# Performance work log

Measured on AMD Instinct MI355X. Metric: run time of the kernel, lower is better.

The kernel has to match this reference:

```python
import jax, jax.numpy as jnp
import numpy as np
import math

HIDDEN = 2048
N_HEADS = 16
HEAD_DIM = HIDDEN // N_HEADS  # 128
ROPE_THETA = 10000.0


def _rope_cos_sin(seq_len, dim, theta, dtype):
    # Megatron RotaryEmbedding: freqs = pos \outer inv_freq; emb = cat(freqs, freqs)
    inv_freq = 1.0 / (theta ** (jnp.arange(0, dim, 2, dtype=jnp.float32) / dim))
    pos = jnp.arange(seq_len, dtype=jnp.float32)
    freqs = jnp.outer(pos, inv_freq)            # [S, dim/2]
    emb = jnp.concatenate([freqs, freqs], -1)   # [S, dim]
    return jnp.cos(emb).astype(dtype), jnp.sin(emb).astype(dtype)


def _rotate_half(x):
    half = x.shape[-1] // 2
    return jnp.concatenate([-x[..., half:], x[..., :half]], axis=-1)


def setup_inputs() -> dict:
    key = jax.random.key(0)
    k1, k2, k3 = jax.random.split(key, 3)
    B, S = 2, 2048
    hidden_states = jax.random.normal(k1, (B, S, HIDDEN), dtype=jnp.float32)
    # torch Linear weights are [out_features, in_features]
    w_qkv = jax.random.normal(k2, (3 * HIDDEN, HIDDEN), dtype=jnp.float32) * (1.0 / math.sqrt(HIDDEN))
    w_o = jax.random.normal(k3, (HIDDEN, HIDDEN), dtype=jnp.float32) * (1.0 / math.sqrt(HIDDEN))
    return {"hidden_states": hidden_states, "w_qkv": w_qkv, "w_o": w_o}


def reference(hidden_states, w_qkv, w_o):
    B, S, H = hidden_states.shape
    # fused QKV projection: [B,S,H] @ [H, 3H] -> view (.., n_heads, 3, head_dim)
    mixed = jnp.einsum('bsh,oh->bso', hidden_states, w_qkv)
    mixed = mixed.reshape(B, S, N_HEADS, 3, HEAD_DIM)
    q, k, v = mixed[..., 0, :], mixed[..., 1, :], mixed[..., 2, :]  # [B,S,Hn,D]

    # fused split + RoPE (full rotary dim = head_dim)
    cos, sin = _rope_cos_sin(S, HEAD_DIM, ROPE_THETA, hidden_states.dtype)
    cos = cos[None, :, None, :]  # [1,S,1,D]
    sin = sin[None, :, None, :]
    q = q * cos + _rotate_half(q) * sin
    k = k * cos + _rotate_half(k) * sin

    # causal scaled-dot-product attention (flash_attn_func equivalent math)
    scale = 1.0 / math.sqrt(HEAD_DIM)
    scores = jnp.einsum('bqhd,bkhd->bhqk', q, k) * scale  # [B,Hn,S,S]
    causal = jnp.tril(jnp.ones((S, S), dtype=bool))
    scores = jnp.where(causal[None, None], scores, jnp.finfo(scores.dtype).min)
    probs = jax.nn.softmax(scores, axis=-1)
    attn = jnp.einsum('bhqk,bkhd->bqhd', probs, v)  # [B,S,Hn,D]

    attn = attn.reshape(B, S, H)
    out = jnp.einsum('bsh,oh->bso', attn, w_o)
    return out
```

## Files before the change

kernel.cpp:

```cpp
#include <hip/hip_runtime.h>
#include <hip/hip_bf16.h>
#include <cstdint>
#include <cstddef>

#define S_DIM 2048
#define H_DIM 2048
#define NHEAD 16
#define HD_DIM 128
#define O3    6144
#define BS    4096
#define NBH   32

typedef short  s16x4  __attribute__((ext_vector_type(4)));
typedef short  s16x8  __attribute__((ext_vector_type(8)));
typedef __bf16 bf16x8 __attribute__((ext_vector_type(8)));
typedef float  f32x4  __attribute__((ext_vector_type(4)));

__device__ __forceinline__ unsigned short f2bf(float f) {
  unsigned int b = __float_as_uint(f);
  b += 0x7FFFu + ((b >> 16) & 1u);
  return (unsigned short)(b >> 16);
}
__device__ __forceinline__ float bf2f(unsigned short u) {
  return __uint_as_float(((unsigned int)u) << 16);
}
__device__ __forceinline__ bf16x8 load8(const unsigned short* p) {
  s16x8 r = *(const s16x8*)p;
  return __builtin_bit_cast(bf16x8, r);
}
__device__ __forceinline__ f32x4 mfma_bf16(bf16x8 a, bf16x8 b, f32x4 c) {
  return __builtin_amdgcn_mfma_f32_16x16x32_bf16(a, b, c, 0, 0, 0);
}
__device__ __forceinline__ void gload_lds16(const void* g, void* l) {
  __builtin_amdgcn_global_load_lds(
      (__attribute__((address_space(1))) unsigned int*)g,
      (__attribute__((address_space(3))) unsigned int*)l, 16, 0, 0);
}

__global__ void prep_kernel(const float* __restrict__ hid,
                            const float* __restrict__ wqkv,
                            const float* __restrict__ wo,
                            unsigned short* __restrict__ hid_b,
                            unsigned short* __restrict__ wqkv_b,
                            unsigned short* __restrict__ wo_b,
                            float* __restrict__ cosT,
                            float* __restrict__ sinT) {
  const int nA = 2097152, nB = 3145728, nC = 1048576, nD = 131072;
  const int total = nA + nB + nC + nD;
  int stride = gridDim.x * blockDim.x;
  for (int i = blockIdx.x * blockDim.x + threadIdx.x; i < total; i += stride) {
    if (i < nA + nB + nC) {
      const float* src; unsigned short* dst; int j;
      if (i < nA)            { src = hid;  dst = hid_b;  j = i; }
      else if (i < nA + nB)  { src = wqkv; dst = wqkv_b; j = i - nA; }
      else                   { src = wo;   dst = wo_b;   j = i - nA - nB; }
      float4 v = ((const float4*)src)[j];
      ushort4 o;
      o.x = f2bf(v.x); o.y = f2bf(v.y); o.z = f2bf(v.z); o.w = f2bf(v.w);
      ((ushort4*)dst)[j] = o;
    } else {
      int idx = i - nA - nB - nC;
      int s = idx >> 6, d = idx & 63;
      float inv = expf(-((float)d / 64.0f) * 9.210340371976184f);
      float ang = (float)s * inv;
      float sn, cs;
      sincosf(ang, &sn, &cs);
      cosT[idx] = cs;
      sinT[idx] = sn;
    }
  }
}

template <bool OUT_BF16, bool QKV_MAP>
__global__ __launch_bounds__(512, 1)
void gemm3b_kernel(const unsigned short* __restrict__ A,
                   const unsigned short* __restrict__ Bw,
                   void* __restrict__ C, int M, int N, int K) {
  __shared__ __align__(16) unsigned short lA[3][128 * 64];
  __shared__ __align__(16) unsigned short lB[3][256 * 64];
  const int tid  = threadIdx.x;
  const int wave = tid >> 6, lane = tid & 63;
  const int wm = wave >> 2, wn = wave & 3;
  const int lg = lane >> 4, ll = lane & 15;

  const int nbx = gridDim.x;
  const int id  = blockIdx.y * nbx + blockIdx.x;
  int m_tile, n_tile;
  if (QKV_MAP) {
    const int k = id & 7, q = id >> 3;
    const int ng = q >> 5, r = q & 31;
    m_tile = (k >> 1) * 8 + (r & 7);
    n_tile = (k & 1) * 12 + ng * 4 + (r >> 3);
  } else {
    const int nwg = gridDim.x * gridDim.y;
    const int swz = (id & 7) * (nwg >> 3) + (id >> 3);
    m_tile = swz / nbx;
    n_tile = swz % nbx;
  }
  const int m0 = m_tile * 128, n0 = n_tile * 256;

  f32x4 acc[4][4];
#pragma unroll
  for (int i = 0; i < 4; ++i)
#pragma unroll
    for (int j = 0; j < 4; ++j) acc[i][j] = (f32x4){0.f, 0.f, 0.f, 0.f};

  const unsigned short* aP[2];
  const unsigned short* bP[4];
  int aD[2], bD[4];
#pragma unroll
  for (int i = 0; i < 2; ++i) {
    int cb = (i * 8 + wave) * 64 + lane;
    int cs = cb ^ ((cb >> 3) & 7);
    aP[i] = A + (size_t)(m0 + (cs >> 3)) * K + (cs & 7) * 8;
    aD[i] = cb * 8;
  }
#pragma unroll
  for (int i = 0; i < 4; ++i) {
    int cb = (i * 8 + wave) * 64 + lane;
    int cs = cb ^ ((cb >> 3) & 7);
    bP[i] = Bw + (size_t)(n0 + (cs >> 3)) * K + (cs & 7) * 8;
    bD[i] = cb * 8;
  }

  auto STAGE = [&](int buf, int t) {
    const int kt = t << 6;
#pragma unroll
    for (int i = 0; i < 2; ++i) gload_lds16(aP[i] + kt, &lA[buf][aD[i]]);
#pragma unroll
    for (int i = 0; i < 4; ++i) gload_lds16(bP[i] + kt, &lB[buf][bD[i]]);
  };

  const int NT = K >> 6;
  STAGE(0, 0);
  if (NT > 1) {
    STAGE(1, 1);
    asm volatile("s_waitcnt vmcnt(6)" ::: "memory");
  } else {
    asm volatile("s_waitcnt vmcnt(0)" ::: "memory");
  }
  asm volatile("s_barrier" ::: "memory");

  for (int t = 0; t < NT; ++t) {
    const int cur = t % 3;
    const char* lAc = (const char*)&lA[cur][0];
    const char* lBc = (const char*)&lB[cur][0];

    bf16x8 af[4][2], bfr[2][2][2];
#pragma unroll
    for (int fq = 0; fq < 4; ++fq) {
      int r = wm * 64 + fq * 16 + ll;
#pragma unroll
      for (int kk = 0; kk < 2; ++kk) {
        int a = (r * 128 + kk * 64 + lg * 16) ^ ((r & 7) << 4);
        af[fq][kk] = load8((const unsigned short*)(lAc + a));
      }
    }
#pragma unroll
    for (int nh = 0; nh < 2; ++nh)
#pragma unroll
      for (int fq = 0; fq < 2; ++fq) {
        int r = wn * 64 + nh * 32 + fq * 16 + ll;
#pragma unroll
        for (int kk = 0; kk < 2; ++kk) {
          int a = (r * 128 + kk * 64 + lg * 16) ^ ((r & 7) << 4);
          bfr[nh][fq][kk] = load8((const unsigned short*)(lBc + a));
        }
      }

    if (t + 2 < NT) STAGE((t + 2) % 3, t + 2);

    __builtin_amdgcn_s_setprio(1);
#pragma unroll
    for (int nh = 0; nh < 2; ++nh)
#pragma unroll
      for (int fq = 0; fq < 4; ++fq)
#pragma unroll
        for (int gq = 0; gq < 2; ++gq)
#pragma unroll
          for (int kk = 0; kk < 2; ++kk)
            acc[fq][nh * 2 + gq] =
                mfma_bf16(af[fq][kk], bfr[nh][gq][kk], acc[fq][nh * 2 + gq]);
    __builtin_amdgcn_s_setprio(0);

    if (t + 2 < NT)
      asm volatile("s_waitcnt vmcnt(6)" ::: "memory");
    else if (t + 1 < NT)
      asm volatile("s_waitcnt vmcnt(0)" ::: "memory");
    asm volatile("s_barrier" ::: "memory");
  }

#pragma unroll
  for (int fm = 0; fm < 4; ++fm)
#pragma unroll
    for (int fn = 0; fn < 4; ++fn)
#pragma unroll
      for (int j = 0; j < 4; ++j) {
        int r   = m0 + wm * 64 + fm * 16 + lg * 4 + j;
        int col = n0 + wn * 64 + fn * 16 + ll;
        if (OUT_BF16)
          ((unsigned short*)C)[(size_t)r * N + col] = f2bf(acc[fm][fn][j]);
        else
          ((float*)C)[(size_t)r * N + col] = acc[fm][fn][j];
      }
}

__global__ void rope_qk_kernel(const unsigned short* __restrict__ mixed,
                               const float* __restrict__ cosT,
                               const float* __restrict__ sinT,
                               unsigned short* __restrict__ qr,
                               unsigned short* __restrict__ kr) {
  int m = blockIdx.x;
  int s = m & (S_DIM - 1);
  int b = m >> 11;
  const unsigned short* row = mixed + (size_t)m * O3;
  int t = threadIdx.x;
  int h = t >> 4, dg = (t & 15) << 2;
  int base = h * 384;
  s16x4 q0 = *(const s16x4*)(row + base + dg);
  s16x4 q1 = *(const s16x4*)(row + base + 64 + dg);
  s16x4 k0 = *(const s16x4*)(row + base + 128 + dg);
  s16x4 k1 = *(const s16x4*)(row + base + 192 + dg);
  float4 c4 = *(const float4*)(cosT + (s << 6) + dg);
  float4 s4 = *(const float4*)(sinT + (s << 6) + dg);
  size_t ob = ((size_t)(b * NHEAD + h) * S_DIM + s) * HD_DIM;
  s16x4 oq0, oq1, ok0, ok1;
  float cc[4] = {c4.x, c4.y, c4.z, c4.w};
  float ss[4] = {s4.x, s4.y, s4.z, s4.w};
#pragma unroll
  for (int i = 0; i < 4; ++i) {
    float q0f = bf2f((unsigned short)q0[i]), q1f = bf2f((unsigned short)q1[i]);
    float k0f = bf2f((unsigned short)k0[i]), k1f = bf2f((unsigned short)k1[i]);
    oq0[i] = (short)f2bf(q0f * cc[i] - q1f * ss[i]);
    oq1[i] = (short)f2bf(q1f * cc[i] + q0f * ss[i]);
    ok0[i] = (short)f2bf(k0f * cc[i] - k1f * ss[i]);
    ok1[i] = (short)f2bf(k1f * cc[i] + k0f * ss[i]);
  }
  *(s16x4*)(qr + ob + dg)      = oq0;
  *(s16x4*)(qr + ob + 64 + dg) = oq1;
  *(s16x4*)(kr + ob + dg)      = ok0;
  *(s16x4*)(kr + ob + 64 + dg) = ok1;
}

__global__ __launch_bounds__(256)
void vtrans_kernel(const unsigned short* __restrict__ mixed,
                   unsigned short* __restrict__ vt) {
  __shared__ unsigned short t[64 * 65];
  int st = blockIdx.x, dt = blockIdx.y, bh = blockIdx.z;
  int b = bh >> 4, h = bh & 15;
  int s0 = st * 64, d0 = dt * 64;
  int tid = threadIdx.x;
#pragma unroll
  for (int it = 0; it < 2; ++it) {
    int c = it * 256 + tid;
    int sl = c >> 3, dc = c & 7;
    const unsigned short* src =
        mixed + (size_t)(b * S_DIM + s0 + sl) * O3 + h * 384 + 256 + d0 + dc * 8;
    s16x8 v = *(const s16x8*)src;
#pragma unroll
    for (int i = 0; i < 8; ++i) t[(dc * 8 + i) * 65 + sl] = (unsigned short)v[i];
  }
  __syncthreads();
#pragma unroll
  for (int it = 0; it < 2; ++it) {
    int c = it * 256 + tid;
    int dl = c >> 3, sc = c & 7;
    s16x8 v;
#pragma unroll
    for (int i = 0; i < 8; ++i) v[i] = (short)t[dl * 65 + sc * 8 + i];
    *(s16x8*)(vt + ((size_t)bh * HD_DIM + d0 + dl) * S_DIM + s0 + sc * 8) = v;
  }
}

__global__ __launch_bounds__(256, 2)
void attn_kernel(const unsigned short* __restrict__ qr,
                 const unsigned short* __restrict__ kr,
                 const unsigned short* __restrict__ vt,
                 unsigned short* __restrict__ out) {
  __shared__ __align__(16) unsigned short kbuf[2][64 * 128];
  __shared__ __align__(16) unsigned short vbuf[2][128 * 64];
  __shared__ __align__(16) unsigned short plds[4][16 * 72];
  const int p = blockIdx.x, bh = blockIdx.y;
  const int wave = threadIdx.x >> 6, lane = threadIdx.x & 63;
  const int b = bh >> 4, h = bh & 15;
  const int lg = lane >> 4, ll = lane & 15;
  const unsigned short* Qb = qr + (size_t)bh * S_DIM * HD_DIM;
  const unsigned short* Kb = kr + (size_t)bh * S_DIM * HD_DIM;
  const unsigned short* Vb = vt + (size_t)bh * HD_DIM * S_DIM;
  const float kE  = 0.12752792f;
  const float THR = 11.5416f;
  unsigned short* pw = &plds[wave][0];

  for (int seg = 0; seg < 2; ++seg) {
    const int qt = seg ? (31 - p) : p;
    const int qbase = qt * 64 + wave * 16;
    const int ntb = qt + 1;

    auto STAGE = [&](int buf, int t) {
      const int k0 = t * 64;
#pragma unroll
      for (int i = 0; i < 4; ++i) {
        int cb = (i * 4 + wave) * 64;
        int c  = cb + lane;
        int cs = c ^ ((c >> 4) & 7);
        gload_lds16(Kb + (size_t)(k0 + (cs >> 4)) * HD_DIM + (cs & 15) * 8,
                    &kbuf[buf][cb * 8]);
      }
#pragma unroll
      for (int i = 0; i < 4; ++i) {
        int cb = (i * 4 + wave) * 64;
        int c  = cb + lane;
        int cv = c ^ ((c >> 3) & 7);
        gload_lds16(Vb + (size_t)(cv >> 3) * S_DIM + k0 + (cv & 7) * 8,
                    &vbuf[buf][cb * 8]);
      }
    };

    bf16x8 aq[4];
#pragma unroll
    for (int kk = 0; kk < 4; ++kk)
      aq[kk] = load8(Qb + (size_t)(qbase + ll) * HD_DIM + kk * 32 + lg * 8);

    float mk[4], lsum[4];
    f32x4 o[8];
#pragma unroll
    for (int j = 0; j < 4; ++j) { mk[j] = -1e30f; lsum[j] = 0.f; }
#pragma unroll
    for (int f = 0; f < 8; ++f) o[f] = (f32x4){0.f, 0.f, 0.f, 0.f};

    STAGE(0, 0);
    __syncthreads();

    for (int t = 0; t < ntb; ++t) {
      const int cur = t & 1;
      if (t + 1 < ntb) STAGE(cur ^ 1, t + 1);
      const int k0 = t * 64;
      const bool diag = (t == ntb - 1);

      f32x4 s[4];
#pragma unroll
      for (int kf = 0; kf < 4; ++kf) s[kf] = (f32x4){0.f, 0.f, 0.f, 0.f};
      const char* kb = (const char*)&kbuf[cur][0];
      __builtin_amdgcn_s_setprio(1);
#pragma unroll
      for (int kf = 0; kf < 4; ++kf) {
        int r = kf * 16 + ll;
#pragma unroll
        for (int kk = 0; kk < 4; ++kk) {
          int a = (r * 256 + kk * 64 + lg * 16) ^ ((r & 7) << 4);
          s[kf] = mfma_bf16(aq[kk], load8((const unsigned short*)(kb + a)), s[kf]);
        }
      }
      __builtin_amdgcn_s_setprio(0);

      if (diag) {
#pragma unroll
        for (int kf = 0; kf < 4; ++kf) {
          int kcol = k0 + kf * 16 + ll;
#pragma unroll
          for (int j = 0; j < 4; ++j) {
            int qrow = qbase + lg * 4 + j;
            if (kcol > qrow) s[kf][j] = -1e31f;
          }
        }
      }

      float pmax[4];
      bool ok = true;
#pragma unroll
      for (int j = 0; j < 4; ++j) {
        pmax[j] = fmaxf(fmaxf(s[0][j], s[1][j]), fmaxf(s[2][j], s[3][j]));
        ok = ok && (pmax[j] * kE - mk[j] <= THR);
      }
      if (!__all(ok)) {
#pragma unroll
        for (int j = 0; j < 4; ++j) {
          float rm = pmax[j] * kE;
#pragma unroll
          for (int off = 1; off < 16; off <<= 1)
            rm = fmaxf(rm, __shfl_xor(rm, off, 64));
          rm = fmaxf(rm, mk[j]);
          float corr = exp2f(mk[j] - rm);
          mk[j] = rm;
          lsum[j] *= corr;
#pragma unroll
          for (int f = 0; f < 8; ++f) o[f][j] *= corr;
        }
      }
#pragma unroll
      for (int j = 0; j < 4; ++j) {
        int prow = (lg * 4 + j) * 72;
#pragma unroll
        for (int kf = 0; kf < 4; ++kf) {
          float e = exp2f(fmaf(s[kf][j], kE, -mk[j]));
          lsum[j] += e;
          pw[prow + kf * 16 + ll] = f2bf(e);
        }
      }

      bf16x8 pa0 = load8(&pw[ll * 72 + lg * 8]);
      bf16x8 pa1 = load8(&pw[ll * 72 + 32 + lg * 8]);
      const char* vb = (const char*)&vbuf[cur][0];
      __builtin_amdgcn_s_setprio(1);
#pragma unroll
      for (int f = 0; f < 8; ++f) {
        int rv = f * 16 + ll;
        int a0 = (rv * 128 + lg * 16) ^ ((rv & 7) << 4);
        int a1 = (rv * 128 + 64 + lg * 16) ^ ((rv & 7) << 4);
        o[f] = mfma_bf16(pa0, load8((const unsigned short*)(vb + a0)), o[f]);
        o[f] = mfma_bf16(pa1, load8((const unsigned short*)(vb + a1)), o[f]);
      }
      __builtin_amdgcn_s_setprio(0);

      __syncthreads();
    }

#pragma unroll
    for (int j = 0; j < 4; ++j) {
      float l = lsum[j];
#pragma unroll
      for (int off = 1; off < 16; off <<= 1) l += __shfl_xor(l, off, 64);
      lsum[j] = 1.0f / l;
    }
#pragma unroll
    for (int f = 0; f < 8; ++f)
#pragma unroll
      for (int j = 0; j < 4; ++j) {
        int srow = qbase + lg * 4 + j;
        out[((size_t)(b * S_DIM + srow)) * H_DIM + h * HD_DIM + f * 16 + ll] =
            f2bf(o[f][j] * lsum[j]);
      }
  }
}

extern "C" void kernel_launch(void* const* d_in, const int* in_sizes, int n_in,
                              void* d_out, int out_size, void* d_ws, size_t ws_size,
                              hipStream_t stream) {
  (void)in_sizes; (void)n_in; (void)out_size; (void)ws_size;
  const float* hidden = (const float*)d_in[0];
  const float* wqkv   = (const float*)d_in[1];
  const float* wo     = (const float*)d_in[2];
  char* ws = (char*)d_ws;
  unsigned short* hid_b  = (unsigned short*)(ws);
  unsigned short* wqkv_b = (unsigned short*)(ws + 16777216);
  unsigned short* wo_b   = (unsigned short*)(ws + 41943040);
  unsigned short* mixed  = (unsigned short*)(ws + 50331648);
  unsigned short* q_r    = (unsigned short*)(ws + 100663296);
  unsigned short* k_r    = (unsigned short*)(ws + 117440512);
  unsigned short* v_t    = (unsigned short*)(ws + 134217728);
  unsigned short* attn   = (unsigned short*)(ws + 150994944);
  float* cosT            = (float*)(ws + 167772160);
  float* sinT            = (float*)(ws + 168296448);

  prep_kernel<<<2048, 256, 0, stream>>>(hidden, wqkv, wo, hid_b, wqkv_b, wo_b,
                                        cosT, sinT);

  gemm3b_kernel<true, true><<<dim3(O3 / 256, BS / 128), 512, 0, stream>>>(
      hid_b, wqkv_b, mixed, BS, O3, H_DIM);

  rope_qk_kernel<<<BS, 256, 0, stream>>>(mixed, cosT, sinT, q_r, k_r);
  vtrans_kernel<<<dim3(32, 2, 32), 256, 0, stream>>>(mixed, v_t);

  attn_kernel<<<dim3(16, 32), 256, 0, stream>>>(q_r, k_r, v_t, attn);

  gemm3b_kernel<false, false><<<dim3(H_DIM / 256, BS / 128), 512, 0, stream>>>(
      attn, wo_b, d_out, BS, H_DIM, H_DIM);
}
```

Before: 267.4 us.

## Use 256x256-tile double-buffered GEMM kernel for QKV projection

Adds a new GEMM kernel with 256x256 output tiles (each wave computes 128x64), double-buffered LDS staging with XOR swizzle, an XCD-style block swizzle and s_setprio around the MFMA blocks. It replaces the 128x256 triple-buffered kernel for the QKV projection. The aim is more data reuse per loaded tile and less global traffic. In exchange the grid has only 384 workgroups, register pressure is higher with 32 accumulators per thread, and the pipeline is shallower.

```diff
diff --git a/kernel.cpp b/kernel.cpp
--- a/kernel.cpp
+++ b/kernel.cpp
@@ -71,6 +71,110 @@
   }
 }
 
+__global__ __launch_bounds__(512, 1)
+void gemm256_kernel(const unsigned short* __restrict__ A,
+                    const unsigned short* __restrict__ Bw,
+                    unsigned short* __restrict__ C, int M, int N, int K) {
+  __shared__ __align__(16) unsigned short lA[2][256 * 64];
+  __shared__ __align__(16) unsigned short lB[2][256 * 64];
+  const int tid  = threadIdx.x;
+  const int wave = tid >> 6, lane = tid & 63;
+  const int wm = wave >> 2, wn = wave & 3;
+  const int lg = lane >> 4, ll = lane & 15;
+
+  const int nbx = gridDim.x;
+  const int nwg = gridDim.x * gridDim.y;
+  const int id  = blockIdx.y * nbx + blockIdx.x;
+  const int swz = (id & 7) * (nwg >> 3) + (id >> 3);
+  const int m0 = (swz / nbx) * 256, n0 = (swz % nbx) * 256;
+
+  f32x4 acc[8][4];
+#pragma unroll
+  for (int i = 0; i < 8; ++i)
+#pragma unroll
+    for (int j = 0; j < 4; ++j) acc[i][j] = (f32x4){0.f, 0.f, 0.f, 0.f};
+
+  const unsigned short* aP[4];
+  const unsigned short* bP[4];
+  int aD[4], bD[4];
+#pragma unroll
+  for (int i = 0; i < 4; ++i) {
+    int cb = i * 512 + tid;
+    int cs = cb ^ ((cb >> 3) & 7);
+    aP[i] = A + (size_t)(m0 + (cs >> 3)) * K + (cs & 7) * 8;
+    bP[i] = Bw + (size_t)(n0 + (cs >> 3)) * K + (cs & 7) * 8;
+    aD[i] = cb * 8;
+    bD[i] = cb * 8;
+  }
+
+  auto STAGE = [&](int buf, int t) {
+    const int kt = t << 6;
+#pragma unroll
+    for (int i = 0; i < 4; ++i) gload_lds16(aP[i] + kt, &lA[buf][aD[i]]);
+#pragma unroll
+    for (int i = 0; i < 4; ++i) gload_lds16(bP[i] + kt, &lB[buf][bD[i]]);
+  };
+
+  const int NT = K >> 6;
+  STAGE(0, 0);
+  asm volatile("s_waitcnt vmcnt(0)" ::: "memory");
+  asm volatile("s_barrier" ::: "memory");
+
+  for (int t = 0; t < NT; ++t) {
+    const int cur = t & 1;
+    if (t + 1 < NT) STAGE(cur ^ 1, t + 1);
+
+    const char* lAc = (const char*)&lA[cur][0];
+    const char* lBc = (const char*)&lB[cur][0];
+
+    bf16x8 bfr[4][2];
+#pragma unroll
+    for (int fr = 0; fr < 4; ++fr) {
+      int r = wn * 64 + fr * 16 + ll;
+#pragma unroll
+      for (int kk = 0; kk < 2; ++kk) {
+        int a = (r * 128 + kk * 64 + lg * 16) ^ ((r & 7) << 4);
+        bfr[fr][kk] = load8((const unsigned short*)(lBc + a));
+      }
+    }
+
+#pragma unroll
+    for (int mh = 0; mh < 2; ++mh)
+#pragma unroll
+      for (int kk = 0; kk < 2; ++kk) {
+        bf16x8 af[4];
+#pragma unroll
+        for (int fq = 0; fq < 4; ++fq) {
+          int r = wm * 128 + mh * 64 + fq * 16 + ll;
+          int a = (r * 128 + kk * 64 + lg * 16) ^ ((r & 7) << 4);
+          af[fq] = load8((const unsigned short*)(lAc + a));
+        }
+        __builtin_amdgcn_s_setprio(1);
+#pragma unroll
+        for (int fq = 0; fq < 4; ++fq)
+#pragma unroll
+          for (int fr = 0; fr < 4; ++fr)
+            acc[mh * 4 + fq][fr] =
+                mfma_bf16(af[fq], bfr[fr][kk], acc[mh * 4 + fq][fr]);
+        __builtin_amdgcn_s_setprio(0);
+      }
+
+    if (t + 1 < NT) asm volatile("s_waitcnt vmcnt(0)" ::: "memory");
+    asm volatile("s_barrier" ::: "memory");
+  }
+
+#pragma unroll
+  for (int fm = 0; fm < 8; ++fm)
+#pragma unroll
+    for (int fn = 0; fn < 4; ++fn)
+#pragma unroll
+      for (int j = 0; j < 4; ++j) {
+        int r   = m0 + wm * 128 + fm * 16 + lg * 4 + j;
+        int col = n0 + wn * 64 + fn * 16 + ll;
+        C[(size_t)r * N + col] = f2bf(acc[fm][fn][j]);
+      }
+}
+
 template <bool OUT_BF16, bool QKV_MAP>
 __global__ __launch_bounds__(512, 1)
 void gemm3b_kernel(const unsigned short* __restrict__ A,
@@ -455,7 +559,7 @@
   prep_kernel<<<2048, 256, 0, stream>>>(hidden, wqkv, wo, hid_b, wqkv_b, wo_b,
                                         cosT, sinT);
 
-  gemm3b_kernel<true, true><<<dim3(O3 / 256, BS / 128), 512, 0, stream>>>(
+  gemm256_kernel<<<dim3(O3 / 256, BS / 256), 512, 0, stream>>>(
       hid_b, wqkv_b, mixed, BS, O3, H_DIM);
 
   rope_qk_kernel<<<BS, 256, 0, stream>>>(mixed, cosT, sinT, q_r, k_r);
```

Result: slower. 301.7 us (+12.8%).
